# Kernel tuning notes

Hardware: AMD Instinct MI355X
Metric: run time of the kernel (lower is better)

The kernel has to match this reference:

```python
import jax, jax.numpy as jnp
import numpy as np
from jax import lax

N_EMBED, N_HEAD, N_EXPERTS, TOP_K = 1024, 16, 8, 2
D_FF = 4 * N_EMBED
HEAD = N_EMBED // N_HEAD
LN_EPS = 1e-5


def _layernorm(x, gamma, beta):
    mu = jnp.mean(x, axis=-1, keepdims=True)
    var = jnp.var(x, axis=-1, keepdims=True)
    return (x - mu) * lax.rsqrt(var + LN_EPS) * gamma + beta


def setup_inputs() -> dict:
    key = jax.random.key(0)
    ks = jax.random.split(key, 16)
    B, T = 2, 2048
    s = 0.02
    return {
        "x": jax.random.normal(ks[0], (B, T, N_EMBED), jnp.float32),
        "noise": jax.random.normal(ks[1], (B, T, N_EXPERTS), jnp.float32),
        "gamma1": jnp.ones((N_EMBED,), jnp.float32),
        "beta1": jnp.zeros((N_EMBED,), jnp.float32),
        "gamma2": jnp.ones((N_EMBED,), jnp.float32),
        "beta2": jnp.zeros((N_EMBED,), jnp.float32),
        "w_qkv": jax.random.normal(ks[2], (N_EMBED, 3 * N_EMBED), jnp.float32) * s,
        "w_out": jax.random.normal(ks[3], (N_EMBED, N_EMBED), jnp.float32) * s,
        "w_route": jax.random.normal(ks[4], (N_EMBED, N_EXPERTS), jnp.float32) * s,
        "b_route": jnp.zeros((N_EXPERTS,), jnp.float32),
        "w_noise": jax.random.normal(ks[5], (N_EMBED, N_EXPERTS), jnp.float32) * s,
        "b_noise": jnp.zeros((N_EXPERTS,), jnp.float32),
        "w1": jax.random.normal(ks[6], (N_EXPERTS, N_EMBED, D_FF), jnp.float32) * s,
        "b1": jnp.zeros((N_EXPERTS, D_FF), jnp.float32),
        "w2": jax.random.normal(ks[7], (N_EXPERTS, D_FF, N_EMBED), jnp.float32) * s,
        "b2": jnp.zeros((N_EXPERTS, N_EMBED), jnp.float32),
    }


def _attention(h, w_qkv, w_out):
    B, T, C = h.shape
    qkv = (h @ w_qkv).reshape(B, T, 3, N_HEAD, HEAD)
    q, k, v = qkv[:, :, 0], qkv[:, :, 1], qkv[:, :, 2]  # (B,T,H,hd)
    scores = jnp.einsum("bthd,bshd->bhts", q, k) / jnp.sqrt(jnp.float32(HEAD))
    attn = jax.nn.softmax(scores, axis=-1)
    out = jnp.einsum("bhts,bshd->bthd", attn, v)  # (B,T,H,hd)
    # faithful reproduction of the original permute/reshape/permute sequence
    out = jnp.transpose(out, (0, 2, 1, 3)).reshape(B, C, T)
    out = jnp.transpose(out, (0, 2, 1))  # (B,T,C)
    return out @ w_out


def _sparse_moe(h, noise, w_route, b_route, w_noise, b_noise, w1, b1, w2, b2):
    B, T, C = h.shape
    N = B * T
    flat = h.reshape(N, C)
    logits = flat @ w_route + b_route
    noise_logits = flat @ w_noise + b_noise
    noisy = logits + noise.reshape(N, N_EXPERTS) * jax.nn.softplus(noise_logits)
    full_probs = jax.nn.softmax(noisy, axis=-1)
    top_vals, top_idx = lax.top_k(noisy, TOP_K)  # (N,k)
    gates = jax.nn.softmax(top_vals, axis=-1)
    dense_gates = jnp.zeros((N, N_EXPERTS), flat.dtype).at[
        jnp.arange(N)[:, None], top_idx
    ].set(gates)
    cap = (N * TOP_K) // N_EXPERTS  # expert capacity, capacity_factor=1.0
    updates = jnp.zeros_like(flat)
    for i in range(N_EXPERTS):
        mask = (top_idx == i).any(axis=-1)  # (N,)
        order = jnp.argsort((~mask).astype(jnp.int32), stable=True)
        idx = order[:cap]
        valid = mask[idx]
        xi = flat[idx]  # (cap,C)
        hid = jax.nn.relu(xi @ w1[i] + b1[i])
        yo = hid @ w2[i] + b2[i]
        g = dense_gates[idx, i] * valid.astype(flat.dtype)
        updates = updates.at[idx].add(yo * g[:, None])
    moe_out = updates.reshape(B, T, C)
    entropy = -jnp.sum(full_probs * jnp.log(full_probs + 1e-8), axis=-1)
    return moe_out, entropy.mean()


def reference(x, noise, gamma1, beta1, gamma2, beta2, w_qkv, w_out,
              w_route, b_route, w_noise, b_noise, w1, b1, w2, b2):
    x = x + _attention(_layernorm(x, gamma1, beta1), w_qkv, w_out)
    moe_out, entropy_loss = _sparse_moe(_layernorm(x, gamma2, beta2), noise,
                                        w_route, b_route, w_noise, b_noise,
                                        w1, b1, w2, b2)
    return x + moe_out, entropy_loss
```

## Files before the change

kernel.cpp:

```cpp
#include <hip/hip_runtime.h>
#include <hip/hip_bf16.h>


#define TT   2048
#define NTOK 4096
#define CE   1024
#define DFF  4096
#define NE   8
#define CAP  1024

typedef __bf16 bf16;
typedef __attribute__((ext_vector_type(8))) bf16 bf16x8;
typedef __attribute__((ext_vector_type(4))) bf16 bf16x4;
typedef __attribute__((ext_vector_type(4))) float f32x4;

typedef __attribute__((address_space(1))) const void* as1_t;
typedef __attribute__((address_space(3))) void* as3_t;
__device__ __forceinline__ void gll16(const void* g, void* l) {
  __builtin_amdgcn_global_load_lds((as1_t)g, (as3_t)l, 16, 0, 0);
}

__device__ __forceinline__ void split2(float v, bf16& h, bf16& l) {
  h = (bf16)v;
  l = (bf16)(v - (float)h);
}

template <bool LO>
__global__ __launch_bounds__(256) void wsplit_k(const float* __restrict__ W,
                                                bf16* __restrict__ Th,
                                                bf16* __restrict__ Tl,
                                                int K, int N, long sW, long sT) {
  __shared__ float tile[64][65];
  const int e = blockIdx.z;
  const float* Wb = W + (long)e * sW;
  bf16* Thb = Th + (long)e * sT;
  bf16* Tlb = LO ? Tl + (long)e * sT : nullptr;
  const int k0 = blockIdx.y * 64, n0 = blockIdx.x * 64;
  const int tx = threadIdx.x & 15, ty = threadIdx.x >> 4;
#pragma unroll
  for (int i = 0; i < 4; i++) {
    int kk = ty + i * 16;
    float4 v = *(const float4*)&Wb[(long)(k0 + kk) * N + n0 + tx * 4];
    tile[kk][tx * 4 + 0] = v.x;
    tile[kk][tx * 4 + 1] = v.y;
    tile[kk][tx * 4 + 2] = v.z;
    tile[kk][tx * 4 + 3] = v.w;
  }
  __syncthreads();
#pragma unroll
  for (int i = 0; i < 4; i++) {
    int nn = ty + i * 16;
    bf16x4 hv, lv;
#pragma unroll
    for (int j = 0; j < 4; j++) {
      float v = tile[tx * 4 + j][nn];
      bf16 h, l;
      split2(v, h, l);
      hv[j] = h;
      lv[j] = l;
    }
    long o = (long)(n0 + nn) * K + k0 + tx * 4;
    *(bf16x4*)(Thb + o) = hv;
    if (LO) *(bf16x4*)(Tlb + o) = lv;
  }
}

__global__ __launch_bounds__(256) void vsplit_k(const float* __restrict__ V,
                                                bf16* __restrict__ Th,
                                                bf16* __restrict__ Tl) {
  __shared__ float tile[64][65];
  const int b = blockIdx.z;
  const int vd0 = blockIdx.x * 64, t0 = blockIdx.y * 64;
  const int tx = threadIdx.x & 15, ty = threadIdx.x >> 4;
#pragma unroll
  for (int i = 0; i < 4; i++) {
    int tt = ty + i * 16;
    float4 v = *(const float4*)&V[((long)b * TT + t0 + tt) * 1024 + vd0 + tx * 4];
    tile[tt][tx * 4 + 0] = v.x;
    tile[tt][tx * 4 + 1] = v.y;
    tile[tt][tx * 4 + 2] = v.z;
    tile[tt][tx * 4 + 3] = v.w;
  }
  __syncthreads();
#pragma unroll
  for (int i = 0; i < 4; i++) {
    int vd = ty + i * 16;
    bf16x4 hv, lv;
#pragma unroll
    for (int j = 0; j < 4; j++) {
      float v = tile[tx * 4 + j][vd];
      bf16 h, l;
      split2(v, h, l);
      hv[j] = h;
      lv[j] = l;
    }
    long o = ((long)b * 1024 + vd0 + vd) * (long)TT + t0 + tx * 4;
    *(bf16x4*)(Th + o) = hv;
    *(bf16x4*)(Tl + o) = lv;
  }
}

__global__ __launch_bounds__(256) void ln_k(const float* __restrict__ in,
                                            const float* __restrict__ g,
                                            const float* __restrict__ b,
                                            float* __restrict__ outf,
                                            bf16* __restrict__ outh,
                                            bf16* __restrict__ outl,
                                            float* __restrict__ zp) {
  int row = blockIdx.x, tid = threadIdx.x;
  if (zp && row == 0 && tid < 64) zp[tid] = 0.f;
  const float* xr = in + (long)row * CE;
  float v[4];
  float s = 0.f, s2 = 0.f;
#pragma unroll
  for (int i = 0; i < 4; i++) {
    v[i] = xr[tid + 256 * i];
    s += v[i];
    s2 += v[i] * v[i];
  }
#pragma unroll
  for (int o = 32; o; o >>= 1) {
    s += __shfl_xor(s, o);
    s2 += __shfl_xor(s2, o);
  }
  __shared__ float rs[4], rs2[4];
  int w = tid >> 6, lane = tid & 63;
  if (lane == 0) { rs[w] = s; rs2[w] = s2; }
  __syncthreads();
  s = rs[0] + rs[1] + rs[2] + rs[3];
  s2 = rs2[0] + rs2[1] + rs2[2] + rs2[3];
  float mu = s * (1.f / CE);
  float var = s2 * (1.f / CE) - mu * mu;
  float rstd = rsqrtf(var + 1e-5f);
  long rb = (long)row * CE;
#pragma unroll
  for (int i = 0; i < 4; i++) {
    int c = tid + 256 * i;
    float y = (v[i] - mu) * rstd * g[c] + b[c];
    if (outf) outf[rb + c] = y;
    bf16 h, l;
    split2(y, h, l);
    outh[rb + c] = h;
    outl[rb + c] = l;
  }
}

template <int NPASS, int EPI, bool AGATHER, int TM>
__global__ __launch_bounds__(256, 2) void gemm_k(
    const bf16* __restrict__ Ah, const bf16* __restrict__ Al,
    const bf16* __restrict__ BTh, const bf16* __restrict__ BTl,
    void* __restrict__ O0, void* __restrict__ O1, void* __restrict__ O2,
    int M, int N, int K, const float* __restrict__ resid,
    const float* __restrict__ bias, const int* __restrict__ tokens,
    const int* __restrict__ counts, const float* __restrict__ gslot,
    long sA, long sBT, long sC, int sBias, const bf16* __restrict__ zp) {
  constexpr int NS = (NPASS > 1) ? 2 : 1;
  constexpr int MI = TM / 32;
  constexpr int AISS = TM / 64;
  __shared__ bf16 As[NS][TM * 32];
  __shared__ bf16 Bs[NS][128 * 32];
  const int e = blockIdx.z;
  const int n0 = blockIdx.x * 128, m0 = blockIdx.y * TM;
  const int tid = threadIdx.x;
  const int w = tid >> 6, lane = tid & 63, lm = lane & 15, qd = lane >> 4;
  const int wm = (w & 1) * (TM / 2), wn = (w >> 1) * 64;

  const bf16* Ab = Ah + (long)e * sA;
  const bf16* AbL = (NS > 1) ? Al + (long)e * sA : nullptr;
  const bf16* Bb = BTh + (long)e * sBT;
  const bf16* BbL = (NS > 1) ? BTl + (long)e * sBT : nullptr;

  const int kc = (lane & 3) * 8;
  int cnt = 0;
  if (AGATHER || EPI == 3) cnt = counts[e];

  const bf16* aP[AISS];
  const bf16* aPL[AISS];
  int aStep[AISS];
  int ldsA[AISS];
#pragma unroll
  for (int ii = 0; ii < AISS; ii++) {
    int sr = w * (TM / 4) + ii * 16 + (lane >> 2);
    ldsA[ii] = (w * TM + ii * 64) * 8;
    aStep[ii] = 32;
    if (AGATHER) {
      int gm = m0 + sr;
      int tk = (gm < cnt) ? tokens[e * CAP + gm] : -1;
      if (tk < 0) { aP[ii] = (const bf16*)zp + kc; aStep[ii] = 0; }
      else aP[ii] = Ab + (long)tk * K + kc;
    } else {
      aP[ii] = Ab + (long)(m0 + sr) * K + kc;
    }
    aPL[ii] = (NS > 1) ? AbL + (aP[ii] - Ab) : nullptr;
  }
  const bf16* bP[2];
  const bf16* bPL[2];
  int ldsB[2];
#pragma unroll
  for (int ii = 0; ii < 2; ii++) {
    int sr = w * 32 + ii * 16 + (lane >> 2);
    ldsB[ii] = (w * 128 + ii * 64) * 8;
    bP[ii] = Bb + (long)(n0 + sr) * K + kc;
    bPL[ii] = (NS > 1) ? BbL + (bP[ii] - Bb) : nullptr;
  }

  f32x4 acc[MI][4];
#pragma unroll
  for (int i = 0; i < MI; i++)
#pragma unroll
    for (int j = 0; j < 4; j++) acc[i][j] = (f32x4){0.f, 0.f, 0.f, 0.f};

  for (int k0 = 0; k0 < K; k0 += 32) {
#pragma unroll
    for (int ii = 0; ii < AISS; ii++) {
      gll16(aP[ii], (char*)&As[0][0] + ldsA[ii] * 2);
      if (NS > 1) gll16(aPL[ii], (char*)&As[1][0] + ldsA[ii] * 2);
      aP[ii] += aStep[ii];
      if (NS > 1) aPL[ii] += aStep[ii];
    }
#pragma unroll
    for (int ii = 0; ii < 2; ii++) {
      gll16(bP[ii], (char*)&Bs[0][0] + ldsB[ii] * 2);
      if (NS > 1) gll16(bPL[ii], (char*)&Bs[1][0] + ldsB[ii] * 2);
      bP[ii] += 32;
      if (NS > 1) bPL[ii] += 32;
    }
    __syncthreads();
    bf16x8 af[NS][MI], bfv[NS][4];
#pragma unroll
    for (int j = 0; j < 4; j++)
#pragma unroll
      for (int s = 0; s < NS; s++)
        bfv[s][j] = *(const bf16x8*)&Bs[s][(wn + j * 16 + lm) * 32 + qd * 8];
#pragma unroll
    for (int i = 0; i < MI; i++)
#pragma unroll
      for (int s = 0; s < NS; s++)
        af[s][i] = *(const bf16x8*)&As[s][(wm + i * 16 + lm) * 32 + qd * 8];
#pragma unroll
    for (int i = 0; i < MI; i++)
#pragma unroll
      for (int j = 0; j < 4; j++) {
        acc[i][j] = __builtin_amdgcn_mfma_f32_16x16x32_bf16(
            af[0][i], bfv[0][j], acc[i][j], 0, 0, 0);
        if (NPASS > 1) {
          acc[i][j] = __builtin_amdgcn_mfma_f32_16x16x32_bf16(
              af[0][i], bfv[1][j], acc[i][j], 0, 0, 0);
          acc[i][j] = __builtin_amdgcn_mfma_f32_16x16x32_bf16(
              af[1][i], bfv[0][j], acc[i][j], 0, 0, 0);
        }
      }
    __syncthreads();
  }
#pragma unroll
  for (int i = 0; i < MI; i++)
#pragma unroll
    for (int j = 0; j < 4; j++) {
      long row = m0 + wm + i * 16 + qd * 4;
      long col = n0 + wn + j * 16 + lm;
      if (EPI == 0) {
        if (col < 2048) {
          bf16* qh = (bf16*)O0;
          bf16* ql = (bf16*)O1;
#pragma unroll
          for (int r = 0; r < 4; r++) {
            bf16 h, l;
            split2(acc[i][j][r], h, l);
            qh[(row + r) * 2048 + col] = h;
            ql[(row + r) * 2048 + col] = l;
          }
        } else {
          float* vt = (float*)O2;
          long vd = col - 2048;
#pragma unroll
          for (int r = 0; r < 4; r++) vt[(row + r) * 1024 + vd] = acc[i][j][r];
        }
      } else if (EPI == 1) {
        float* outp = (float*)O0;
#pragma unroll
        for (int r = 0; r < 4; r++)
          outp[(row + r) * N + col] = resid[(row + r) * N + col] + acc[i][j][r];
      } else if (EPI == 2) {
        bf16* hid = (bf16*)O0;
        float bv = bias[e * sBias + col];
#pragma unroll
        for (int r = 0; r < 4; r++) {
          float t = acc[i][j][r] + bv;
          hid[(long)e * sC + (row + r) * (long)N + col] =
              (bf16)(t > 0.f ? t : 0.f);
        }
      } else {
        float* outp = (float*)O0;
        float bv = bias[e * sBias + col];
#pragma unroll
        for (int r = 0; r < 4; r++) {
          long rr = row + r;
          if (rr < cnt) {
            int tok = tokens[e * CAP + rr];
            float gv = gslot[e * CAP + rr];
            atomicAdd(&outp[(long)tok * CE + col], gv * (acc[i][j][r] + bv));
          }
        }
      }
    }
}

__global__ __launch_bounds__(256, 2) void attn_k(
    const bf16* __restrict__ qkvh, const bf16* __restrict__ qkvl,
    const bf16* __restrict__ VTh, const bf16* __restrict__ VTl,
    bf16* __restrict__ attn_h, bf16* __restrict__ attn_l) {
  const int qt = blockIdx.x, h = blockIdx.y, b = blockIdx.z;
  const int tid = threadIdx.x, w = tid >> 6, lane = tid & 63;
  const int lm = lane & 15, qd = lane >> 4;
  __shared__ bf16 Ks[2][64 * 64];
  __shared__ bf16 Vs[2][64 * 64];
  __shared__ bf16 Ps[4][2][32][72];
  const long bb = (long)b * TT;

  bf16x8 qfh[2][2], qfl[2][2];
#pragma unroll
  for (int i = 0; i < 2; i++) {
    long qrow = (bb + qt * 128 + w * 32 + i * 16 + lm) * 2048 + h * 64;
#pragma unroll
    for (int kk = 0; kk < 2; kk++) {
      qfh[i][kk] = *(const bf16x8*)(qkvh + qrow + kk * 32 + qd * 8);
      qfl[i][kk] = *(const bf16x8*)(qkvl + qrow + kk * 32 + qd * 8);
    }
  }

  const int ktok = tid >> 3, dc = tid & 7;
  const int kws = ktok * 64 + ((dc ^ (ktok & 7)) * 8);
  const long gK0 = (bb + ktok) * 2048 + 1024 + h * 64 + dc * 8;
  const int vd = tid >> 3, tc = tid & 7;
  const int vws = vd * 64 + ((tc ^ (vd & 7)) * 8);
  const long gV0 = ((long)b * 1024 + h * 64 + vd) * (long)TT + tc * 8;

  const bf16* pKh = qkvh + gK0;
  const bf16* pKl = qkvl + gK0;
  const bf16* pVh = VTh + gV0;
  const bf16* pVl = VTl + gV0;

  float4 rkh0, rkh1, rkl0, rkl1, rvh0, rvh1, rvl0, rvl1;
#define LOADT()                               \
  do {                                        \
    rkh0 = *(const float4*)(pKh);             \
    rkh1 = *(const float4*)(pKh + 32 * 2048); \
    rkl0 = *(const float4*)(pKl);             \
    rkl1 = *(const float4*)(pKl + 32 * 2048); \
    rvh0 = *(const float4*)(pVh);             \
    rvh1 = *(const float4*)(pVh + 32 * TT);   \
    rvl0 = *(const float4*)(pVl);             \
    rvl1 = *(const float4*)(pVl + 32 * TT);   \
  } while (0)
  LOADT();

  float l_lane[2][4];
  f32x4 o[2][4];
#pragma unroll
  for (int i = 0; i < 2; i++)
#pragma unroll
    for (int r = 0; r < 4; r++) l_lane[i][r] = 0.f;
#pragma unroll
  for (int i = 0; i < 2; i++)
#pragma unroll
    for (int nt = 0; nt < 4; nt++) o[i][nt] = (f32x4){0.f, 0.f, 0.f, 0.f};

  const float SC = 0.125f * 1.4426950408889634f;

  for (int kt = 0; kt < TT / 64; kt++) {
    __syncthreads();
    *(float4*)&Ks[0][kws] = rkh0;
    *(float4*)&Ks[0][kws + 32 * 64] = rkh1;
    *(float4*)&Ks[1][kws] = rkl0;
    *(float4*)&Ks[1][kws + 32 * 64] = rkl1;
    *(float4*)&Vs[0][vws] = rvh0;
    *(float4*)&Vs[0][vws + 32 * 64] = rvh1;
    *(float4*)&Vs[1][vws] = rvl0;
    *(float4*)&Vs[1][vws + 32 * 64] = rvl1;
    if (kt != TT / 64 - 1) {
      pKh += 64 * 2048; pKl += 64 * 2048; pVh += 64; pVl += 64;
      LOADT();
    }
    __syncthreads();
    f32x4 sv[2][4];
#pragma unroll
    for (int i = 0; i < 2; i++)
#pragma unroll
      for (int nt = 0; nt < 4; nt++) sv[i][nt] = (f32x4){0.f, 0.f, 0.f, 0.f};
#pragma unroll
    for (int nt = 0; nt < 4; nt++) {
      int tok = nt * 16 + lm;
#pragma unroll
      for (int kk = 0; kk < 2; kk++) {
        int slot = ((kk * 4 + qd) ^ (lm & 7)) * 8;
        bf16x8 kh = *(const bf16x8*)&Ks[0][tok * 64 + slot];
        bf16x8 kl = *(const bf16x8*)&Ks[1][tok * 64 + slot];
#pragma unroll
        for (int i = 0; i < 2; i++) {
          sv[i][nt] = __builtin_amdgcn_mfma_f32_16x16x32_bf16(qfh[i][kk], kh,
                                                              sv[i][nt], 0, 0, 0);
          sv[i][nt] = __builtin_amdgcn_mfma_f32_16x16x32_bf16(qfh[i][kk], kl,
                                                              sv[i][nt], 0, 0, 0);
          sv[i][nt] = __builtin_amdgcn_mfma_f32_16x16x32_bf16(qfl[i][kk], kh,
                                                              sv[i][nt], 0, 0, 0);
        }
      }
    }
#pragma unroll
    for (int i = 0; i < 2; i++)
#pragma unroll
      for (int nt = 0; nt < 4; nt++)
#pragma unroll
        for (int r = 0; r < 4; r++) {
          float p = __builtin_exp2f(sv[i][nt][r] * SC);
          l_lane[i][r] += p;
          bf16 hh, ll;
          split2(p, hh, ll);
          Ps[w][0][i * 16 + qd * 4 + r][nt * 16 + lm] = hh;
          Ps[w][1][i * 16 + qd * 4 + r][nt * 16 + lm] = ll;
        }
#pragma unroll
    for (int kcl = 0; kcl < 2; kcl++) {
      bf16x8 ph[2], pl[2];
#pragma unroll
      for (int i = 0; i < 2; i++) {
        ph[i] = *(const bf16x8*)&Ps[w][0][i * 16 + lm][kcl * 32 + qd * 8];
        pl[i] = *(const bf16x8*)&Ps[w][1][i * 16 + lm][kcl * 32 + qd * 8];
      }
#pragma unroll
      for (int nt = 0; nt < 4; nt++) {
        int drow = nt * 16 + lm;
        int slot = ((kcl * 4 + qd) ^ (lm & 7)) * 8;
        bf16x8 vh = *(const bf16x8*)&Vs[0][drow * 64 + slot];
        bf16x8 vl = *(const bf16x8*)&Vs[1][drow * 64 + slot];
#pragma unroll
        for (int i = 0; i < 2; i++) {
          o[i][nt] = __builtin_amdgcn_mfma_f32_16x16x32_bf16(ph[i], vh, o[i][nt], 0, 0, 0);
          o[i][nt] = __builtin_amdgcn_mfma_f32_16x16x32_bf16(ph[i], vl, o[i][nt], 0, 0, 0);
          o[i][nt] = __builtin_amdgcn_mfma_f32_16x16x32_bf16(pl[i], vh, o[i][nt], 0, 0, 0);
        }
      }
    }
  }
#pragma unroll
  for (int i = 0; i < 2; i++)
#pragma unroll
    for (int r = 0; r < 4; r++)
#pragma unroll
      for (int d = 8; d; d >>= 1) l_lane[i][r] += __shfl_xor(l_lane[i][r], d);
#pragma unroll
  for (int i = 0; i < 2; i++)
#pragma unroll
    for (int nt = 0; nt < 4; nt++)
#pragma unroll
      for (int r = 0; r < 4; r++) {
        int t = qt * 128 + w * 32 + i * 16 + qd * 4 + r;
        int d = nt * 16 + lm;
        int ttn = (t & 31) * 64 + d;
        int c = h * 64 + (t >> 5);
        float v = o[i][nt][r] / l_lane[i][r];
        bf16 hh, ll;
        split2(v, hh, ll);
        long idx = (bb + ttn) * (long)CE + c;
        attn_h[idx] = hh;
        attn_l[idx] = ll;
      }
#undef LOADT
}

__global__ __launch_bounds__(64) void route_k(
    const float* __restrict__ hln, const float* __restrict__ noise,
    const float* __restrict__ wr, const float* __restrict__ br,
    const float* __restrict__ wn, const float* __restrict__ bn,
    int* __restrict__ top_e, float* __restrict__ gates,
    float* __restrict__ entb) {
  int n = blockIdx.x, lane = threadIdx.x;
  const float* hr = hln + (long)n * CE;
  float aR[NE], aN[NE];
#pragma unroll
  for (int e = 0; e < NE; e++) { aR[e] = 0.f; aN[e] = 0.f; }
  for (int i = lane; i < CE; i += 64) {
    float hv = hr[i];
#pragma unroll
    for (int e = 0; e < NE; e++) {
      aR[e] += hv * wr[i * NE + e];
      aN[e] += hv * wn[i * NE + e];
    }
  }
#pragma unroll
  for (int e = 0; e < NE; e++)
#pragma unroll
    for (int d = 32; d; d >>= 1) {
      aR[e] += __shfl_xor(aR[e], d);
      aN[e] += __shfl_xor(aN[e], d);
    }
  if (lane == 0) {
    float ns[NE];
#pragma unroll
    for (int e = 0; e < NE; e++) {
      float lg = aR[e] + br[e];
      float nl = aN[e] + bn[e];
      float sp = (nl > 20.f) ? nl : log1pf(expf(nl));
      ns[e] = lg + noise[(long)n * NE + e] * sp;
    }
    int i0 = 0;
#pragma unroll
    for (int e = 1; e < NE; e++)
      if (ns[e] > ns[i0]) i0 = e;
    int i1 = (i0 == 0) ? 1 : 0;
#pragma unroll
    for (int e = 0; e < NE; e++)
      if (e != i0 && ns[e] > ns[i1]) i1 = e;
    float v0 = ns[i0], v1 = ns[i1];
    float e1v = expf(v1 - v0);
    float inv2 = 1.f / (1.f + e1v);
    top_e[2 * n] = i0;
    top_e[2 * n + 1] = i1;
    gates[2 * n] = inv2;
    gates[2 * n + 1] = e1v * inv2;
    float ssum = 0.f, p[NE];
#pragma unroll
    for (int e = 0; e < NE; e++) {
      p[e] = expf(ns[e] - v0);
      ssum += p[e];
    }
    float is = 1.f / ssum, ent = 0.f;
#pragma unroll
    for (int e = 0; e < NE; e++) {
      float pe = p[e] * is;
      ent -= pe * logf(pe + 1e-8f);
    }
    entb[n] = ent;
  }
}

__global__ __launch_bounds__(256) void assign_k(const int* __restrict__ top_e,
                                                const float* __restrict__ gates,
                                                int* __restrict__ tokens,
                                                float* __restrict__ gslot,
                                                int* __restrict__ counts) {
  int e = blockIdx.x, tid = threadIdx.x, w = tid >> 6, lane = tid & 63;
  __shared__ int wtot[4];
  int basec = 0;
  for (int c = 0; c < 16; c++) {
    int n = c * 256 + tid;
    int e0 = top_e[2 * n], e1 = top_e[2 * n + 1];
    bool flag = (e0 == e) || (e1 == e);
    int rank = (e0 == e) ? 0 : 1;
    unsigned long long mask = __ballot(flag);
    int pre = __popcll(mask & ((1ull << lane) - 1ull));
    if (lane == 0) wtot[w] = __popcll(mask);
    __syncthreads();
    int wbase = basec;
    for (int i = 0; i < w; i++) wbase += wtot[i];
    if (flag) {
      int slot = wbase + pre;
      if (slot < CAP) {
        tokens[e * CAP + slot] = n;
        gslot[e * CAP + slot] = gates[2 * n + rank];
      }
    }
    int tot = wtot[0] + wtot[1] + wtot[2] + wtot[3];
    __syncthreads();
    basec += tot;
  }
  if (tid == 0) counts[e] = basec < CAP ? basec : CAP;
}

__global__ __launch_bounds__(256) void entropy_k(const float* __restrict__ entb,
                                                 float* __restrict__ outp) {
  int tid = threadIdx.x;
  float s = 0.f;
  for (int i = tid; i < NTOK; i += 256) s += entb[i];
#pragma unroll
  for (int d = 32; d; d >>= 1) s += __shfl_xor(s, d);
  __shared__ float rs[4];
  int w = tid >> 6, lane = tid & 63;
  if (lane == 0) rs[w] = s;
  __syncthreads();
  if (tid == 0)
    outp[(long)NTOK * CE] = (rs[0] + rs[1] + rs[2] + rs[3]) * (1.f / NTOK);
}

extern "C" void kernel_launch(void* const* d_in, const int* in_sizes, int n_in,
                              void* d_out, int out_size, void* d_ws,
                              size_t ws_size, hipStream_t stream) {
  const float* x = (const float*)d_in[0];
  const float* noise = (const float*)d_in[1];
  const float* gamma1 = (const float*)d_in[2];
  const float* beta1 = (const float*)d_in[3];
  const float* gamma2 = (const float*)d_in[4];
  const float* beta2 = (const float*)d_in[5];
  const float* w_qkv = (const float*)d_in[6];
  const float* w_out = (const float*)d_in[7];
  const float* w_route = (const float*)d_in[8];
  const float* b_route = (const float*)d_in[9];
  const float* w_noise = (const float*)d_in[10];
  const float* b_noise = (const float*)d_in[11];
  const float* w1 = (const float*)d_in[12];
  const float* b1 = (const float*)d_in[13];
  const float* w2 = (const float*)d_in[14];
  const float* b2 = (const float*)d_in[15];
  float* out = (float*)d_out;

  char* ws = (char*)d_ws;
  size_t offA = 0;
  bf16* qkvh = (bf16*)(ws + offA);  offA += (size_t)NTOK * 2048 * 2;
  bf16* qkvl = (bf16*)(ws + offA);  offA += (size_t)NTOK * 2048 * 2;
  bf16* VTh = (bf16*)(ws + offA);   offA += (size_t)2 * 1024 * TT * 2;
  bf16* VTl = (bf16*)(ws + offA);   offA += (size_t)2 * 1024 * TT * 2;
  size_t attn_off = offA;
  bf16* attn_h = (bf16*)(ws + offA); offA += (size_t)NTOK * CE * 2;
  bf16* attn_l = (bf16*)(ws + offA); offA += (size_t)NTOK * CE * 2;
  bf16* hid = (bf16*)ws;
  float* vtmp = (float*)(ws + attn_off);
  float* h2f = (float*)(ws + attn_off);
  size_t szA = offA;
  size_t offB = szA;
  bf16* h1h = (bf16*)(ws + offB);    offB += (size_t)NTOK * CE * 2;
  bf16* h1l = (bf16*)(ws + offB);    offB += (size_t)NTOK * CE * 2;
  bf16* wqkvTh = (bf16*)(ws + offB); offB += (size_t)3072 * 1024 * 2;
  bf16* wqkvTl = (bf16*)(ws + offB); offB += (size_t)3072 * 1024 * 2;
  bf16* woutTh = (bf16*)(ws + offB); offB += (size_t)1024 * 1024 * 2;
  bf16* woutTl = (bf16*)(ws + offB); offB += (size_t)1024 * 1024 * 2;
  bf16* h2h = (bf16*)(ws + szA);
  bf16* h2l = (bf16*)(ws + szA + (size_t)NTOK * CE * 2);
  size_t offC = offB;
  bf16* w1T = (bf16*)(ws + offC);
  bf16* w2T = w1T;
  offC += (size_t)NE * DFF * CE * 2;
  size_t offS = offC;
  int* top_e = (int*)(ws + offS);    offS += (size_t)NTOK * 2 * 4;
  float* gates = (float*)(ws + offS); offS += (size_t)NTOK * 2 * 4;
  int* toks = (int*)(ws + offS);     offS += (size_t)NE * CAP * 4;
  float* gslot = (float*)(ws + offS); offS += (size_t)NE * CAP * 4;
  int* counts = (int*)(ws + offS);   offS += 256;
  float* entb = (float*)(ws + offS); offS += (size_t)NTOK * 4;
  float* zp = (float*)(ws + offS);   offS += 256;
  if (offS > ws_size) return;

  wsplit_k<true><<<dim3(48, 16, 1), 256, 0, stream>>>(w_qkv, wqkvTh, wqkvTl,
                                                      1024, 3072, 0, 0);
  wsplit_k<true><<<dim3(16, 16, 1), 256, 0, stream>>>(w_out, woutTh, woutTl,
                                                      1024, 1024, 0, 0);
  wsplit_k<false><<<dim3(64, 16, 8), 256, 0, stream>>>(
      w1, w1T, nullptr, 1024, DFF, (long)CE * DFF, (long)DFF * CE);
  ln_k<<<NTOK, 256, 0, stream>>>(x, gamma1, beta1, nullptr, h1h, h1l, zp);
  gemm_k<3, 0, false, 128><<<dim3(24, 32, 1), 256, 0, stream>>>(
      h1h, h1l, wqkvTh, wqkvTl, qkvh, qkvl, vtmp, NTOK, 3 * CE, CE, nullptr,
      nullptr, nullptr, nullptr, nullptr, 0, 0, 0, 0, (const bf16*)zp);
  vsplit_k<<<dim3(16, 32, 2), 256, 0, stream>>>(vtmp, VTh, VTl);
  attn_k<<<dim3(16, 16, 2), 256, 0, stream>>>(qkvh, qkvl, VTh, VTl, attn_h,
                                              attn_l);
  gemm_k<3, 1, false, 64><<<dim3(8, 64, 1), 256, 0, stream>>>(
      attn_h, attn_l, woutTh, woutTl, out, nullptr, nullptr, NTOK, CE, CE, x,
      nullptr, nullptr, nullptr, nullptr, 0, 0, 0, 0, (const bf16*)zp);
  ln_k<<<NTOK, 256, 0, stream>>>(out, gamma2, beta2, h2f, h2h, h2l, nullptr);
  route_k<<<NTOK, 64, 0, stream>>>(h2f, noise, w_route, b_route, w_noise,
                                   b_noise, top_e, gates, entb);
  assign_k<<<NE, 256, 0, stream>>>(top_e, gates, toks, gslot, counts);
  gemm_k<1, 2, true, 128><<<dim3(DFF / 128, CAP / 128, NE), 256, 0, stream>>>(
      h2h, nullptr, w1T, nullptr, hid, nullptr, nullptr, CAP, DFF, CE, nullptr,
      b1, toks, counts, nullptr, 0, (long)DFF * CE, (long)CAP * DFF, DFF,
      (const bf16*)zp);
  wsplit_k<false><<<dim3(16, 64, 8), 256, 0, stream>>>(
      w2, w2T, nullptr, DFF, CE, (long)DFF * CE, (long)CE * DFF);
  gemm_k<1, 3, false, 128><<<dim3(CE / 128, CAP / 128, NE), 256, 0, stream>>>(
      hid, nullptr, w2T, nullptr, out, nullptr, nullptr, CAP, CE, DFF, nullptr,
      b2, toks, counts, gslot, (long)CAP * DFF, (long)CE * DFF, 0, CE,
      (const bf16*)zp);
  entropy_k<<<1, 256, 0, stream>>>(entb, out);
}
```

Before: 915.9 us.

## Split attention block into 8 waves of 16 query rows each

The attention kernel now launches 512 threads per block, so each of 8 waves handles 16 query rows instead of 32 across 4 waves. Each thread loads one K/V float4 per tile instead of two, the P scratch buffer shrinks and is processed in two 32-key halves, and register use per wave roughly halves, with launch bounds raised to allow more waves per CU. The aim is more latency hiding through occupancy. The cost is that every K/V fragment read from LDS now feeds half as many MFMAs, which doubles LDS read traffic per FLOP, and block-wide syncs now cover more waves.

```diff
diff --git a/kernel.cpp b/kernel.cpp
--- a/kernel.cpp
+++ b/kernel.cpp
@@ -305,7 +305,7 @@
     }
 }
 
-__global__ __launch_bounds__(256, 2) void attn_k(
+__global__ __launch_bounds__(512, 4) void attn_k(
     const bf16* __restrict__ qkvh, const bf16* __restrict__ qkvl,
     const bf16* __restrict__ VTh, const bf16* __restrict__ VTl,
     bf16* __restrict__ attn_h, bf16* __restrict__ attn_l) {
@@ -314,17 +314,16 @@
   const int lm = lane & 15, qd = lane >> 4;
   __shared__ bf16 Ks[2][64 * 64];
   __shared__ bf16 Vs[2][64 * 64];
-  __shared__ bf16 Ps[4][2][32][72];
+  __shared__ bf16 Ps[8][2][16][40];
   const long bb = (long)b * TT;
 
-  bf16x8 qfh[2][2], qfl[2][2];
-#pragma unroll
-  for (int i = 0; i < 2; i++) {
-    long qrow = (bb + qt * 128 + w * 32 + i * 16 + lm) * 2048 + h * 64;
+  bf16x8 qfh[2], qfl[2];
+  {
+    long qrow = (bb + qt * 128 + w * 16 + lm) * 2048 + h * 64;
 #pragma unroll
     for (int kk = 0; kk < 2; kk++) {
-      qfh[i][kk] = *(const bf16x8*)(qkvh + qrow + kk * 32 + qd * 8);
-      qfl[i][kk] = *(const bf16x8*)(qkvl + qrow + kk * 32 + qd * 8);
+      qfh[kk] = *(const bf16x8*)(qkvh + qrow + kk * 32 + qd * 8);
+      qfl[kk] = *(const bf16x8*)(qkvl + qrow + kk * 32 + qd * 8);
     }
   }
 
@@ -340,131 +339,101 @@
   const bf16* pVh = VTh + gV0;
   const bf16* pVl = VTl + gV0;
 
-  float4 rkh0, rkh1, rkl0, rkl1, rvh0, rvh1, rvl0, rvl1;
-#define LOADT()                               \
-  do {                                        \
-    rkh0 = *(const float4*)(pKh);             \
-    rkh1 = *(const float4*)(pKh + 32 * 2048); \
-    rkl0 = *(const float4*)(pKl);             \
-    rkl1 = *(const float4*)(pKl + 32 * 2048); \
-    rvh0 = *(const float4*)(pVh);             \
-    rvh1 = *(const float4*)(pVh + 32 * TT);   \
-    rvl0 = *(const float4*)(pVl);             \
-    rvl1 = *(const float4*)(pVl + 32 * TT);   \
+  float4 rkh, rkl, rvh, rvl;
+#define LOADT()                  \
+  do {                           \
+    rkh = *(const float4*)(pKh); \
+    rkl = *(const float4*)(pKl); \
+    rvh = *(const float4*)(pVh); \
+    rvl = *(const float4*)(pVl); \
   } while (0)
   LOADT();
 
-  float l_lane[2][4];
-  f32x4 o[2][4];
-#pragma unroll
-  for (int i = 0; i < 2; i++)
-#pragma unroll
-    for (int r = 0; r < 4; r++) l_lane[i][r] = 0.f;
-#pragma unroll
-  for (int i = 0; i < 2; i++)
-#pragma unroll
-    for (int nt = 0; nt < 4; nt++) o[i][nt] = (f32x4){0.f, 0.f, 0.f, 0.f};
+  float l_lane[4];
+  f32x4 o[4];
+#pragma unroll
+  for (int r = 0; r < 4; r++) l_lane[r] = 0.f;
+#pragma unroll
+  for (int nt = 0; nt < 4; nt++) o[nt] = (f32x4){0.f, 0.f, 0.f, 0.f};
 
   const float SC = 0.125f * 1.4426950408889634f;
 
   for (int kt = 0; kt < TT / 64; kt++) {
     __syncthreads();
-    *(float4*)&Ks[0][kws] = rkh0;
-    *(float4*)&Ks[0][kws + 32 * 64] = rkh1;
-    *(float4*)&Ks[1][kws] = rkl0;
-    *(float4*)&Ks[1][kws + 32 * 64] = rkl1;
-    *(float4*)&Vs[0][vws] = rvh0;
-    *(float4*)&Vs[0][vws + 32 * 64] = rvh1;
-    *(float4*)&Vs[1][vws] = rvl0;
-    *(float4*)&Vs[1][vws + 32 * 64] = rvl1;
+    *(float4*)&Ks[0][kws] = rkh;
+    *(float4*)&Ks[1][kws] = rkl;
+    *(float4*)&Vs[0][vws] = rvh;
+    *(float4*)&Vs[1][vws] = rvl;
     if (kt != TT / 64 - 1) {
       pKh += 64 * 2048; pKl += 64 * 2048; pVh += 64; pVl += 64;
       LOADT();
     }
     __syncthreads();
-    f32x4 sv[2][4];
-#pragma unroll
-    for (int i = 0; i < 2; i++)
-#pragma unroll
-      for (int nt = 0; nt < 4; nt++) sv[i][nt] = (f32x4){0.f, 0.f, 0.f, 0.f};
-#pragma unroll
-    for (int nt = 0; nt < 4; nt++) {
-      int tok = nt * 16 + lm;
-#pragma unroll
-      for (int kk = 0; kk < 2; kk++) {
-        int slot = ((kk * 4 + qd) ^ (lm & 7)) * 8;
-        bf16x8 kh = *(const bf16x8*)&Ks[0][tok * 64 + slot];
-        bf16x8 kl = *(const bf16x8*)&Ks[1][tok * 64 + slot];
-#pragma unroll
-        for (int i = 0; i < 2; i++) {
-          sv[i][nt] = __builtin_amdgcn_mfma_f32_16x16x32_bf16(qfh[i][kk], kh,
-                                                              sv[i][nt], 0, 0, 0);
-          sv[i][nt] = __builtin_amdgcn_mfma_f32_16x16x32_bf16(qfh[i][kk], kl,
-                                                              sv[i][nt], 0, 0, 0);
-          sv[i][nt] = __builtin_amdgcn_mfma_f32_16x16x32_bf16(qfl[i][kk], kh,
-                                                              sv[i][nt], 0, 0, 0);
+#pragma unroll
+    for (int th = 0; th < 2; th++) {
+      f32x4 sv[2];
+#pragma unroll
+      for (int ntl = 0; ntl < 2; ntl++) sv[ntl] = (f32x4){0.f, 0.f, 0.f, 0.f};
+#pragma unroll
+      for (int ntl = 0; ntl < 2; ntl++) {
+        int tok = (th * 2 + ntl) * 16 + lm;
+#pragma unroll
+        for (int kk = 0; kk < 2; kk++) {
+          int slot = ((kk * 4 + qd) ^ (lm & 7)) * 8;
+          bf16x8 kh = *(const bf16x8*)&Ks[0][tok * 64 + slot];
+          bf16x8 kl = *(const bf16x8*)&Ks[1][tok * 64 + slot];
+          sv[ntl] = __builtin_amdgcn_mfma_f32_16x16x32_bf16(qfh[kk], kh,
+                                                            sv[ntl], 0, 0, 0);
+          sv[ntl] = __builtin_amdgcn_mfma_f32_16x16x32_bf16(qfh[kk], kl,
+                                                            sv[ntl], 0, 0, 0);
+          sv[ntl] = __builtin_amdgcn_mfma_f32_16x16x32_bf16(qfl[kk], kh,
+                                                            sv[ntl], 0, 0, 0);
         }
       }
-    }
-#pragma unroll
-    for (int i = 0; i < 2; i++)
-#pragma unroll
-      for (int nt = 0; nt < 4; nt++)
+#pragma unroll
+      for (int ntl = 0; ntl < 2; ntl++)
 #pragma unroll
         for (int r = 0; r < 4; r++) {
-          float p = __builtin_exp2f(sv[i][nt][r] * SC);
-          l_lane[i][r] += p;
+          float p = __builtin_exp2f(sv[ntl][r] * SC);
+          l_lane[r] += p;
           bf16 hh, ll;
           split2(p, hh, ll);
-          Ps[w][0][i * 16 + qd * 4 + r][nt * 16 + lm] = hh;
-          Ps[w][1][i * 16 + qd * 4 + r][nt * 16 + lm] = ll;
+          Ps[w][0][qd * 4 + r][ntl * 16 + lm] = hh;
+          Ps[w][1][qd * 4 + r][ntl * 16 + lm] = ll;
         }
-#pragma unroll
-    for (int kcl = 0; kcl < 2; kcl++) {
-      bf16x8 ph[2], pl[2];
-#pragma unroll
-      for (int i = 0; i < 2; i++) {
-        ph[i] = *(const bf16x8*)&Ps[w][0][i * 16 + lm][kcl * 32 + qd * 8];
-        pl[i] = *(const bf16x8*)&Ps[w][1][i * 16 + lm][kcl * 32 + qd * 8];
-      }
+      bf16x8 ph = *(const bf16x8*)&Ps[w][0][lm][qd * 8];
+      bf16x8 pl = *(const bf16x8*)&Ps[w][1][lm][qd * 8];
 #pragma unroll
       for (int nt = 0; nt < 4; nt++) {
         int drow = nt * 16 + lm;
-        int slot = ((kcl * 4 + qd) ^ (lm & 7)) * 8;
+        int slot = ((th * 4 + qd) ^ (lm & 7)) * 8;
         bf16x8 vh = *(const bf16x8*)&Vs[0][drow * 64 + slot];
         bf16x8 vl = *(const bf16x8*)&Vs[1][drow * 64 + slot];
-#pragma unroll
-        for (int i = 0; i < 2; i++) {
-          o[i][nt] = __builtin_amdgcn_mfma_f32_16x16x32_bf16(ph[i], vh, o[i][nt], 0, 0, 0);
-          o[i][nt] = __builtin_amdgcn_mfma_f32_16x16x32_bf16(ph[i], vl, o[i][nt], 0, 0, 0);
-          o[i][nt] = __builtin_amdgcn_mfma_f32_16x16x32_bf16(pl[i], vh, o[i][nt], 0, 0, 0);
-        }
+        o[nt] = __builtin_amdgcn_mfma_f32_16x16x32_bf16(ph, vh, o[nt], 0, 0, 0);
+        o[nt] = __builtin_amdgcn_mfma_f32_16x16x32_bf16(ph, vl, o[nt], 0, 0, 0);
+        o[nt] = __builtin_amdgcn_mfma_f32_16x16x32_bf16(pl, vh, o[nt], 0, 0, 0);
       }
     }
   }
 #pragma unroll
-  for (int i = 0; i < 2; i++)
-#pragma unroll
-    for (int r = 0; r < 4; r++)
-#pragma unroll
-      for (int d = 8; d; d >>= 1) l_lane[i][r] += __shfl_xor(l_lane[i][r], d);
-#pragma unroll
-  for (int i = 0; i < 2; i++)
-#pragma unroll
-    for (int nt = 0; nt < 4; nt++)
-#pragma unroll
-      for (int r = 0; r < 4; r++) {
-        int t = qt * 128 + w * 32 + i * 16 + qd * 4 + r;
-        int d = nt * 16 + lm;
-        int ttn = (t & 31) * 64 + d;
-        int c = h * 64 + (t >> 5);
-        float v = o[i][nt][r] / l_lane[i][r];
-        bf16 hh, ll;
-        split2(v, hh, ll);
-        long idx = (bb + ttn) * (long)CE + c;
-        attn_h[idx] = hh;
-        attn_l[idx] = ll;
-      }
+  for (int r = 0; r < 4; r++)
+#pragma unroll
+    for (int d = 8; d; d >>= 1) l_lane[r] += __shfl_xor(l_lane[r], d);
+#pragma unroll
+  for (int nt = 0; nt < 4; nt++)
+#pragma unroll
+    for (int r = 0; r < 4; r++) {
+      int t = qt * 128 + w * 16 + qd * 4 + r;
+      int d = nt * 16 + lm;
+      int ttn = (t & 31) * 64 + d;
+      int c = h * 64 + (t >> 5);
+      float v = o[nt][r] / l_lane[r];
+      bf16 hh, ll;
+      split2(v, hh, ll);
+      long idx = (bb + ttn) * (long)CE + c;
+      attn_h[idx] = hh;
+      attn_l[idx] = ll;
+    }
 #undef LOADT
 }
 
@@ -650,7 +619,7 @@
       h1h, h1l, wqkvTh, wqkvTl, qkvh, qkvl, vtmp, NTOK, 3 * CE, CE, nullptr,
       nullptr, nullptr, nullptr, nullptr, 0, 0, 0, 0, (const bf16*)zp);
   vsplit_k<<<dim3(16, 32, 2), 256, 0, stream>>>(vtmp, VTh, VTl);
-  attn_k<<<dim3(16, 16, 2), 256, 0, stream>>>(qkvh, qkvl, VTh, VTl, attn_h,
+  attn_k<<<dim3(16, 16, 2), 512, 0, stream>>>(qkvh, qkvl, VTh, VTl, attn_h,
                                               attn_l);
   gemm_k<3, 1, false, 64><<<dim3(8, 64, 1), 256, 0, stream>>>(
       attn_h, attn_l, woutTh, woutTl, out, nullptr, nullptr, NTOK, CE, CE, x,
```

Result: no change. 909.7 us (-0.7%).
